# Optimization experiments

Hardware: AMD Instinct MI355X
Metric: run time of the kernel (lower is better)

Reference implementation:

```python
import jax, jax.numpy as jnp
import numpy as np

NEG_INF = -1e9
LEAKY_SLOPE = 0.2


def setup_inputs() -> dict:
    key = jax.random.key(0)
    k1, k2, k3, k4, k5, k6, k7 = jax.random.split(key, 7)
    B, L = 50000, 50          # batch nodes, max padded neighbors (num_sample)
    N = 200000                # unique node embeddings
    D_in, D_out = 256, 64
    padded_neighs = jax.random.randint(k1, (B, L), 0, N, dtype=jnp.int32)
    mask = jax.random.randint(k2, (B, L), 0, 2, dtype=jnp.int32).astype(jnp.bool_)
    mask = mask.at[:, 0].set(True)  # every node has >=1 neighbor
    dst_idx = jax.random.randint(k3, (B,), 0, N, dtype=jnp.int32)
    embed_table = jax.random.normal(k4, (N, D_in), dtype=jnp.float32)
    # xavier_uniform for proj [D_out, D_in]
    bound = float(np.sqrt(6.0 / (D_in + D_out)))
    W_proj = jax.random.uniform(k5, (D_out, D_in), minval=-bound, maxval=bound, dtype=jnp.float32)
    a_src = jax.random.normal(k6, (D_out,), dtype=jnp.float32) * 0.1
    a_dst = jax.random.normal(k7, (D_out,), dtype=jnp.float32) * 0.1
    return {"padded_neighs": padded_neighs, "mask": mask, "dst_idx": dst_idx,
            "embed_table": embed_table, "W_proj": W_proj, "a_src": a_src, "a_dst": a_dst}


def leaky_relu(x):
    return jnp.where(x >= 0, x, LEAKY_SLOPE * x)


def reference(padded_neighs, mask, dst_idx, embed_table, W_proj, a_src, a_dst):
    # project all unique-node embeddings: [N, D_out]
    embed_prime = embed_table @ W_proj.T
    # gather neighbor and dst projected features
    neigh_feats = embed_prime[padded_neighs]          # [B, L, D_out]
    dst_feats = embed_prime[dst_idx]                  # [B, D_out] (constant across L)
    # GAT-style scores: leaky_relu(dst @ a_dst) + leaky_relu(neigh @ a_src)
    dst_attn = leaky_relu(dst_feats @ a_dst)[:, None, None]       # [B, 1, 1]
    neigh_attn = leaky_relu(neigh_feats @ a_src)[:, :, None]      # [B, L, 1]
    edge_attn = dst_attn + neigh_attn                             # [B, L, 1]
    # masked softmax over the neighbor axis
    scores = jnp.where(mask[:, :, None], edge_attn, NEG_INF)
    attn = jax.nn.softmax(scores, axis=1)                         # [B, L, 1]
    # weighted sum of neighbor features
    return jnp.sum(attn * neigh_feats, axis=1)                    # [B, D_out]
```

## Files before the change

### kernel.cpp

```cpp
#include <hip/hip_runtime.h>
#include <stdint.h>

#define DIN 256
#define DOUT 64
#define LMAX 50
#define NEG_INF -1e9f
#define WSTRIDE 264

typedef short bf16x8 __attribute__((ext_vector_type(8)));
typedef float f32x4  __attribute__((ext_vector_type(4)));

static __device__ __forceinline__ unsigned short f2bf(float x) {
    unsigned int u = __float_as_uint(x);
    u += 0x7fffu + ((u >> 16) & 1u);
    return (unsigned short)(u >> 16);
}
static __device__ __forceinline__ float bflo(unsigned int u) { return __uint_as_float(u << 16); }
static __device__ __forceinline__ float bfhi(unsigned int u) { return __uint_as_float(u & 0xffff0000u); }

__global__ __launch_bounds__(256) void proj_kernel(
    const float* __restrict__ embed, const float* __restrict__ W,
    unsigned short* __restrict__ ep16, int N)
{
    __shared__ unsigned short wl[64 * WSTRIDE];

    const int tid  = threadIdx.x;
    const int lane = tid & 63;
    const int wv   = tid >> 6;
    const int mrow = lane & 15;
    const int quad = lane >> 4;

#pragma unroll
    for (int i = 0; i < 16; ++i) {
        const int idx4 = tid + 256 * i;
        const int e    = idx4 * 4;
        const int n    = e >> 8;
        const int k    = e & 255;
        const float4 f = *(const float4*)&W[e];
        union { unsigned short s[4]; unsigned long long v; } p;
        p.s[0] = f2bf(f.x); p.s[1] = f2bf(f.y);
        p.s[2] = f2bf(f.z); p.s[3] = f2bf(f.w);
        *(unsigned long long*)&wl[n * WSTRIDE + k] = p.v;
    }
    __syncthreads();

    const int m_base = blockIdx.x * 128 + wv * 32;

    f32x4 acc[2][4];
#pragma unroll
    for (int mt = 0; mt < 2; ++mt)
#pragma unroll
        for (int nt = 0; nt < 4; ++nt) acc[mt][nt] = (f32x4){0.f, 0.f, 0.f, 0.f};

    for (int kc = 0; kc < DIN; kc += 32) {
        bf16x8 afrag[2];
#pragma unroll
        for (int mt = 0; mt < 2; ++mt) {
            int row = m_base + mt * 16 + mrow;
            if (row >= N) row = N - 1;
            const float* ap = embed + (size_t)row * DIN + kc + quad * 8;
            const float4 f0 = *(const float4*)ap;
            const float4 f1 = *(const float4*)(ap + 4);
            union { short s[8]; bf16x8 f; } a;
            a.s[0] = (short)f2bf(f0.x); a.s[1] = (short)f2bf(f0.y);
            a.s[2] = (short)f2bf(f0.z); a.s[3] = (short)f2bf(f0.w);
            a.s[4] = (short)f2bf(f1.x); a.s[5] = (short)f2bf(f1.y);
            a.s[6] = (short)f2bf(f1.z); a.s[7] = (short)f2bf(f1.w);
            afrag[mt] = a.f;
        }
#pragma unroll
        for (int nt = 0; nt < 4; ++nt) {
            const bf16x8 bfrag =
                *(const bf16x8*)&wl[(nt * 16 + mrow) * WSTRIDE + kc + quad * 8];
            acc[0][nt] = __builtin_amdgcn_mfma_f32_16x16x32_bf16(
                afrag[0], bfrag, acc[0][nt], 0, 0, 0);
            acc[1][nt] = __builtin_amdgcn_mfma_f32_16x16x32_bf16(
                afrag[1], bfrag, acc[1][nt], 0, 0, 0);
        }
    }

#pragma unroll
    for (int mt = 0; mt < 2; ++mt)
#pragma unroll
        for (int nt = 0; nt < 4; ++nt)
#pragma unroll
            for (int r = 0; r < 4; ++r) {
                const int row = m_base + mt * 16 + quad * 4 + r;
                if (row < N)
                    ep16[(size_t)row * DOUT + nt * 16 + mrow] = f2bf(acc[mt][nt][r]);
            }
}

struct NodePrep { bool mvalid; unsigned int du; };

__global__ __launch_bounds__(256) void agg_kernel(
    const int* __restrict__ neighs, const void* __restrict__ mask,
    const int* __restrict__ dst_idx, const unsigned int* __restrict__ ep16u,
    const float* __restrict__ a_src, const float* __restrict__ a_dst,
    float* __restrict__ out, int B)
{
    __shared__ unsigned int fwbuf[4][2][LMAX * 32];
    __shared__ float attn_s[4][64];

    const int tid  = threadIdx.x;
    const int lane = tid & 63;
    const int wv   = tid >> 6;
    const int gw   = blockIdx.x * 4 + wv;
    const int c    = lane & 31;

    const unsigned int* mw = (const unsigned int*)mask;
    const bool byteMode = (mw[12] > 1u);

    const float2 adv = *(const float2*)&a_dst[2 * c];

    const int gchunk = (lane & 7) ^ (lane >> 3);

    auto prep_and_dma = [&](int node, unsigned int* buf) -> NodePrep {
        NodePrep p;
        const int* nb = neighs + (size_t)node * LMAX;
        p.mvalid = false;
        if (lane < LMAX) {
            const int mi = node * LMAX + lane;
            p.mvalid = byteMode ? (((const uint8_t*)mask)[mi] != 0)
                                : (((const int*)mask)[mi] != 0);
        }
        const unsigned long long vm = __ballot(p.mvalid);
        const int n0 = nb[0];
#pragma unroll
        for (int i = 0; i < 6; ++i) {
            const int r = 8 * i + (lane >> 3);
            const int n = ((vm >> r) & 1ull) ? nb[r] : n0;
            const unsigned int* gp = ep16u + (size_t)n * 32 + gchunk * 4;
            __builtin_amdgcn_global_load_lds(
                (const __attribute__((address_space(1))) void*)gp,
                (__attribute__((address_space(3))) void*)&buf[i * 256],
                16, 0, 0);
        }
        {
            const int r  = 48 + (lane >> 5);
            const int n  = ((vm >> r) & 1ull) ? nb[r] : n0;
            const int w  = lane & 31;
            const int gwd = (((w >> 2) ^ (r & 7)) << 2) + (w & 3);
            const unsigned int* gp = ep16u + (size_t)n * 32 + gwd;
            __builtin_amdgcn_global_load_lds(
                (const __attribute__((address_space(1))) void*)gp,
                (__attribute__((address_space(3))) void*)&buf[48 * 32],
                4, 0, 0);
        }
        p.du = ep16u[(size_t)dst_idx[node] * 32 + c];
        return p;
    };

    auto compute_store = [&](int node, const unsigned int* buf, const NodePrep& p) {
        float pd = bflo(p.du) * adv.x + bfhi(p.du) * adv.y;
#pragma unroll
        for (int m = 32; m >= 1; m >>= 1) pd += __shfl_xor(pd, m, 64);
        pd *= 0.5f;
        const float dst_attn = pd >= 0.f ? pd : 0.2f * pd;

        const int l    = lane < LMAX ? lane : 0;
        const int rot7 = l & 7;
        const unsigned int* fr = buf + l * 32;
        float dot = 0.f;
#pragma unroll
        for (int k8 = 0; k8 < 8; ++k8) {
            const uint4 u = *(const uint4*)&fr[((k8 ^ rot7) << 2)];
            dot = fmaf(bflo(u.x), a_src[k8 * 8 + 0], dot);
            dot = fmaf(bfhi(u.x), a_src[k8 * 8 + 1], dot);
            dot = fmaf(bflo(u.y), a_src[k8 * 8 + 2], dot);
            dot = fmaf(bfhi(u.y), a_src[k8 * 8 + 3], dot);
            dot = fmaf(bflo(u.z), a_src[k8 * 8 + 4], dot);
            dot = fmaf(bfhi(u.z), a_src[k8 * 8 + 5], dot);
            dot = fmaf(bflo(u.w), a_src[k8 * 8 + 6], dot);
            dot = fmaf(bfhi(u.w), a_src[k8 * 8 + 7], dot);
        }
        const float lr = dot >= 0.f ? dot : 0.2f * dot;
        float s = (lane < LMAX && p.mvalid) ? (dst_attn + lr) : NEG_INF;

        float mx = s;
#pragma unroll
        for (int m = 32; m >= 1; m >>= 1) mx = fmaxf(mx, __shfl_xor(mx, m, 64));
        const float e = __expf(s - mx);
        float se = e;
#pragma unroll
        for (int m = 32; m >= 1; m >>= 1) se += __shfl_xor(se, m, 64);
        attn_s[wv][lane] = e / se;

        const int half = lane >> 5;
        float acc0 = 0.f, acc1 = 0.f;
#pragma unroll
        for (int i = 0; i < 25; ++i) {
            const int r  = 2 * i + half;
            const int sw = (((c >> 2) ^ (r & 7)) << 2) + (c & 3);
            const unsigned int u = buf[r * 32 + sw];
            const float w = attn_s[wv][r];
            acc0 = fmaf(w, bflo(u), acc0);
            acc1 = fmaf(w, bfhi(u), acc1);
        }
        acc0 += __shfl_xor(acc0, 32, 64);
        acc1 += __shfl_xor(acc1, 32, 64);
        if (lane < 32) {
            float2 o; o.x = acc0; o.y = acc1;
            *(float2*)&out[(size_t)node * DOUT + 2 * c] = o;
        }
    };

    const int b0 = 2 * gw, b1 = 2 * gw + 1;
    const int b0c = b0 < B ? b0 : B - 1;
    const int b1c = b1 < B ? b1 : B - 1;

    NodePrep p0 = prep_and_dma(b0c, &fwbuf[wv][0][0]);
    asm volatile("s_waitcnt vmcnt(0)" ::: "memory");
    NodePrep p1 = prep_and_dma(b1c, &fwbuf[wv][1][0]);
    if (b0 < B) compute_store(b0, &fwbuf[wv][0][0], p0);
    asm volatile("s_waitcnt vmcnt(0)" ::: "memory");
    if (b1 < B) compute_store(b1, &fwbuf[wv][1][0], p1);
}

extern "C" void kernel_launch(void* const* d_in, const int* in_sizes, int n_in,
                              void* d_out, int out_size, void* d_ws, size_t ws_size,
                              hipStream_t stream)
{
    const int*   neighs  = (const int*)d_in[0];
    const void*  mask    = d_in[1];
    const int*   dst_idx = (const int*)d_in[2];
    const float* embed   = (const float*)d_in[3];
    const float* W       = (const float*)d_in[4];
    const float* a_src   = (const float*)d_in[5];
    const float* a_dst   = (const float*)d_in[6];
    float* out = (float*)d_out;

    const int B = in_sizes[2];
    const int N = in_sizes[3] / DIN;

    unsigned short* ep16 = (unsigned short*)d_ws;

    proj_kernel<<<dim3((N + 127) / 128), dim3(256), 0, stream>>>(embed, W, ep16, N);

    const int waves = (B + 1) / 2;
    agg_kernel<<<dim3((waves + 3) / 4), dim3(256), 0, stream>>>(
        neighs, mask, dst_idx, (const unsigned int*)ep16, a_src, a_dst, out, B);
}
```

Baseline: 416.4 us.

## Process one node per wave with a single LDS buffer to raise occupancy

The aggregation kernel now gives each wave one batch node instead of two double-buffered nodes. That halves the per-block LDS footprint and adds a launch-bounds occupancy hint, so more blocks can be resident to hide the latency of the random neighbor gathers. In exchange it gives up the software overlap between one node's DMA and the other node's compute within a wave. It also relies on a block barrier rather than an explicit vmcnt wait to make the LDS data visible, and launches twice as many blocks.

```diff
diff --git a/kernel.cpp b/kernel.cpp
--- a/kernel.cpp
+++ b/kernel.cpp
@@ -91,130 +91,116 @@
             }
 }
 
-struct NodePrep { bool mvalid; unsigned int du; };
-
-__global__ __launch_bounds__(256) void agg_kernel(
+__global__ __launch_bounds__(256, 6) void agg_kernel(
     const int* __restrict__ neighs, const void* __restrict__ mask,
     const int* __restrict__ dst_idx, const unsigned int* __restrict__ ep16u,
     const float* __restrict__ a_src, const float* __restrict__ a_dst,
     float* __restrict__ out, int B)
 {
-    __shared__ unsigned int fwbuf[4][2][LMAX * 32];
+    __shared__ unsigned int fwbuf[4][LMAX * 32];
     __shared__ float attn_s[4][64];
 
     const int tid  = threadIdx.x;
     const int lane = tid & 63;
     const int wv   = tid >> 6;
-    const int gw   = blockIdx.x * 4 + wv;
+    const int b    = blockIdx.x * 4 + wv;
+    const int bc   = b < B ? b : B - 1;
     const int c    = lane & 31;
 
     const unsigned int* mw = (const unsigned int*)mask;
     const bool byteMode = (mw[12] > 1u);
 
+    bool mvalid = false;
+    if (lane < LMAX) {
+        const int mi = bc * LMAX + lane;
+        mvalid = byteMode ? (((const uint8_t*)mask)[mi] != 0)
+                          : (((const int*)mask)[mi] != 0);
+    }
+    const unsigned long long vm = __ballot(mvalid);
+
+    const int* nb = neighs + (size_t)bc * LMAX;
+    const int n0  = nb[0];
+
+    const unsigned int du = ep16u[(size_t)dst_idx[bc] * 32 + c];
     const float2 adv = *(const float2*)&a_dst[2 * c];
 
+    unsigned int* buf = fwbuf[wv];
     const int gchunk = (lane & 7) ^ (lane >> 3);
-
-    auto prep_and_dma = [&](int node, unsigned int* buf) -> NodePrep {
-        NodePrep p;
-        const int* nb = neighs + (size_t)node * LMAX;
-        p.mvalid = false;
-        if (lane < LMAX) {
-            const int mi = node * LMAX + lane;
-            p.mvalid = byteMode ? (((const uint8_t*)mask)[mi] != 0)
-                                : (((const int*)mask)[mi] != 0);
-        }
-        const unsigned long long vm = __ballot(p.mvalid);
-        const int n0 = nb[0];
-#pragma unroll
-        for (int i = 0; i < 6; ++i) {
-            const int r = 8 * i + (lane >> 3);
-            const int n = ((vm >> r) & 1ull) ? nb[r] : n0;
-            const unsigned int* gp = ep16u + (size_t)n * 32 + gchunk * 4;
-            __builtin_amdgcn_global_load_lds(
-                (const __attribute__((address_space(1))) void*)gp,
-                (__attribute__((address_space(3))) void*)&buf[i * 256],
-                16, 0, 0);
-        }
-        {
-            const int r  = 48 + (lane >> 5);
-            const int n  = ((vm >> r) & 1ull) ? nb[r] : n0;
-            const int w  = lane & 31;
-            const int gwd = (((w >> 2) ^ (r & 7)) << 2) + (w & 3);
-            const unsigned int* gp = ep16u + (size_t)n * 32 + gwd;
-            __builtin_amdgcn_global_load_lds(
-                (const __attribute__((address_space(1))) void*)gp,
-                (__attribute__((address_space(3))) void*)&buf[48 * 32],
-                4, 0, 0);
-        }
-        p.du = ep16u[(size_t)dst_idx[node] * 32 + c];
-        return p;
-    };
-
-    auto compute_store = [&](int node, const unsigned int* buf, const NodePrep& p) {
-        float pd = bflo(p.du) * adv.x + bfhi(p.du) * adv.y;
-#pragma unroll
-        for (int m = 32; m >= 1; m >>= 1) pd += __shfl_xor(pd, m, 64);
-        pd *= 0.5f;
-        const float dst_attn = pd >= 0.f ? pd : 0.2f * pd;
-
-        const int l    = lane < LMAX ? lane : 0;
-        const int rot7 = l & 7;
-        const unsigned int* fr = buf + l * 32;
-        float dot = 0.f;
-#pragma unroll
-        for (int k8 = 0; k8 < 8; ++k8) {
-            const uint4 u = *(const uint4*)&fr[((k8 ^ rot7) << 2)];
-            dot = fmaf(bflo(u.x), a_src[k8 * 8 + 0], dot);
-            dot = fmaf(bfhi(u.x), a_src[k8 * 8 + 1], dot);
-            dot = fmaf(bflo(u.y), a_src[k8 * 8 + 2], dot);
-            dot = fmaf(bfhi(u.y), a_src[k8 * 8 + 3], dot);
-            dot = fmaf(bflo(u.z), a_src[k8 * 8 + 4], dot);
-            dot = fmaf(bfhi(u.z), a_src[k8 * 8 + 5], dot);
-            dot = fmaf(bflo(u.w), a_src[k8 * 8 + 6], dot);
-            dot = fmaf(bfhi(u.w), a_src[k8 * 8 + 7], dot);
-        }
-        const float lr = dot >= 0.f ? dot : 0.2f * dot;
-        float s = (lane < LMAX && p.mvalid) ? (dst_attn + lr) : NEG_INF;
-
-        float mx = s;
-#pragma unroll
-        for (int m = 32; m >= 1; m >>= 1) mx = fmaxf(mx, __shfl_xor(mx, m, 64));
-        const float e = __expf(s - mx);
-        float se = e;
-#pragma unroll
-        for (int m = 32; m >= 1; m >>= 1) se += __shfl_xor(se, m, 64);
-        attn_s[wv][lane] = e / se;
-
-        const int half = lane >> 5;
-        float acc0 = 0.f, acc1 = 0.f;
-#pragma unroll
-        for (int i = 0; i < 25; ++i) {
-            const int r  = 2 * i + half;
-            const int sw = (((c >> 2) ^ (r & 7)) << 2) + (c & 3);
-            const unsigned int u = buf[r * 32 + sw];
-            const float w = attn_s[wv][r];
-            acc0 = fmaf(w, bflo(u), acc0);
-            acc1 = fmaf(w, bfhi(u), acc1);
-        }
-        acc0 += __shfl_xor(acc0, 32, 64);
-        acc1 += __shfl_xor(acc1, 32, 64);
-        if (lane < 32) {
-            float2 o; o.x = acc0; o.y = acc1;
-            *(float2*)&out[(size_t)node * DOUT + 2 * c] = o;
-        }
-    };
-
-    const int b0 = 2 * gw, b1 = 2 * gw + 1;
-    const int b0c = b0 < B ? b0 : B - 1;
-    const int b1c = b1 < B ? b1 : B - 1;
-
-    NodePrep p0 = prep_and_dma(b0c, &fwbuf[wv][0][0]);
-    asm volatile("s_waitcnt vmcnt(0)" ::: "memory");
-    NodePrep p1 = prep_and_dma(b1c, &fwbuf[wv][1][0]);
-    if (b0 < B) compute_store(b0, &fwbuf[wv][0][0], p0);
-    asm volatile("s_waitcnt vmcnt(0)" ::: "memory");
-    if (b1 < B) compute_store(b1, &fwbuf[wv][1][0], p1);
+#pragma unroll
+    for (int i = 0; i < 6; ++i) {
+        const int r = 8 * i + (lane >> 3);
+        const int n = ((vm >> r) & 1ull) ? nb[r] : n0;
+        const unsigned int* gp = ep16u + (size_t)n * 32 + gchunk * 4;
+        __builtin_amdgcn_global_load_lds(
+            (const __attribute__((address_space(1))) void*)gp,
+            (__attribute__((address_space(3))) void*)&buf[i * 256],
+            16, 0, 0);
+    }
+    {
+        const int r   = 48 + (lane >> 5);
+        const int n   = ((vm >> r) & 1ull) ? nb[r] : n0;
+        const int w   = lane & 31;
+        const int gwd = (((w >> 2) ^ (r & 7)) << 2) + (w & 3);
+        const unsigned int* gp = ep16u + (size_t)n * 32 + gwd;
+        __builtin_amdgcn_global_load_lds(
+            (const __attribute__((address_space(1))) void*)gp,
+            (__attribute__((address_space(3))) void*)&buf[48 * 32],
+            4, 0, 0);
+    }
+
+    float pd = bflo(du) * adv.x + bfhi(du) * adv.y;
+#pragma unroll
+    for (int m = 32; m >= 1; m >>= 1) pd += __shfl_xor(pd, m, 64);
+    pd *= 0.5f;
+    const float dst_attn = pd >= 0.f ? pd : 0.2f * pd;
+
+    __syncthreads();
+
+    const int l    = lane < LMAX ? lane : 0;
+    const int rot7 = l & 7;
+    const unsigned int* fr = buf + l * 32;
+    float dot = 0.f;
+#pragma unroll
+    for (int k8 = 0; k8 < 8; ++k8) {
+        const uint4 u = *(const uint4*)&fr[((k8 ^ rot7) << 2)];
+        dot = fmaf(bflo(u.x), a_src[k8 * 8 + 0], dot);
+        dot = fmaf(bfhi(u.x), a_src[k8 * 8 + 1], dot);
+        dot = fmaf(bflo(u.y), a_src[k8 * 8 + 2], dot);
+        dot = fmaf(bfhi(u.y), a_src[k8 * 8 + 3], dot);
+        dot = fmaf(bflo(u.z), a_src[k8 * 8 + 4], dot);
+        dot = fmaf(bfhi(u.z), a_src[k8 * 8 + 5], dot);
+        dot = fmaf(bflo(u.w), a_src[k8 * 8 + 6], dot);
+        dot = fmaf(bfhi(u.w), a_src[k8 * 8 + 7], dot);
+    }
+    const float lr = dot >= 0.f ? dot : 0.2f * dot;
+    float s = (lane < LMAX && mvalid) ? (dst_attn + lr) : NEG_INF;
+
+    float mx = s;
+#pragma unroll
+    for (int m = 32; m >= 1; m >>= 1) mx = fmaxf(mx, __shfl_xor(mx, m, 64));
+    const float e = __expf(s - mx);
+    float se = e;
+#pragma unroll
+    for (int m = 32; m >= 1; m >>= 1) se += __shfl_xor(se, m, 64);
+    attn_s[wv][lane] = e / se;
+
+    const int half = lane >> 5;
+    float acc0 = 0.f, acc1 = 0.f;
+#pragma unroll
+    for (int i = 0; i < 25; ++i) {
+        const int r  = 2 * i + half;
+        const int sw = (((c >> 2) ^ (r & 7)) << 2) + (c & 3);
+        const unsigned int u = buf[r * 32 + sw];
+        const float w = attn_s[wv][r];
+        acc0 = fmaf(w, bflo(u), acc0);
+        acc1 = fmaf(w, bfhi(u), acc1);
+    }
+    acc0 += __shfl_xor(acc0, 32, 64);
+    acc1 += __shfl_xor(acc1, 32, 64);
+    if (b < B && lane < 32) {
+        float2 o; o.x = acc0; o.y = acc1;
+        *(float2*)&out[(size_t)b * DOUT + 2 * c] = o;
+    }
 }
 
 extern "C" void kernel_launch(void* const* d_in, const int* in_sizes, int n_in,
@@ -236,8 +222,6 @@
     unsigned short* ep16 = (unsigned short*)d_ws;
 
     proj_kernel<<<dim3((N + 127) / 128), dim3(256), 0, stream>>>(embed, W, ep16, N);
-
-    const int waves = (B + 1) / 2;
-    agg_kernel<<<dim3((waves + 3) / 4), dim3(256), 0, stream>>>(
+    agg_kernel<<<dim3((B + 3) / 4), dim3(256), 0, stream>>>(
         neighs, mask, dst_idx, (const unsigned int*)ep16, a_src, a_dst, out, B);
 }
```

Result: faster. 374.8 us (-10.0%).
